# Optimization experiments

Hardware: AMD Instinct MI355X
Metric: run time of the kernel (lower is better)

Reference implementation:

```python
import jax, jax.numpy as jnp
import numpy as np

TEMP = 0.05
DIAG_PENALTY = 1e12
EPS = 1e-8  # matches torch F.cosine_similarity eps


def setup_inputs() -> dict:
    key = jax.random.key(0)
    x = jax.random.normal(key, (8192, 768), dtype=jnp.float32)
    return {"x": x}


def reference(x):
    n = x.shape[0]
    # labels: swap adjacent pairs -> i - (i%2)*2 + 1  (i.e. i XOR 1)
    idx = jnp.arange(n)
    labels = idx - (idx % 2) * 2 + 1
    # cosine similarity matrix via normalize + GEMM (same math as broadcasted
    # F.cosine_similarity: dot(x_i, x_j) / (max(||x_i||,eps) * max(||x_j||,eps)))
    norms = jnp.maximum(jnp.linalg.norm(x, axis=-1, keepdims=True), EPS)
    xn = x / norms
    sim = xn @ xn.T                                   # [N, N]
    sim = sim - jnp.eye(n, dtype=sim.dtype) * DIAG_PENALTY
    logits = sim / TEMP
    # mean cross-entropy with stable log-softmax
    logp = jax.nn.log_softmax(logits, axis=-1)
    loss = -jnp.mean(jnp.take_along_axis(logp, labels[:, None], axis=-1))
    return loss
```

## Files before the change

### kernel.cpp

```cpp
#include <hip/hip_runtime.h>
#include <hip/hip_bf16.h>

#define N 8192
#define D 768
#define TEMP_INV 20.0f
#define NTILES 2080

typedef __attribute__((ext_vector_type(4))) float f32x4;
typedef __attribute__((ext_vector_type(4))) int i32x4;
typedef __attribute__((ext_vector_type(8))) int i32x8;

#define SCALE1 0x7F7F7F7F


__global__ __launch_bounds__(256) void norm_kernel(
    const float* __restrict__ x, unsigned char* __restrict__ xn,
    float* __restrict__ rowsum) {
  int t = threadIdx.x, w = t >> 6, lane = t & 63;
  int p = blockIdx.x;
  __shared__ unsigned int lds[3072];
#pragma unroll
  for (int it = 0; it < 4; ++it) {
    int r = w * 4 + it;
    const float4* xr = (const float4*)(x + (size_t)(p * 16 + r) * D);
    float4 v[3];
    v[0] = xr[lane];
    v[1] = xr[lane + 64];
    v[2] = xr[lane + 128];
    float ss = 0.0f;
#pragma unroll
    for (int i = 0; i < 3; ++i)
      ss += v[i].x * v[i].x + v[i].y * v[i].y + v[i].z * v[i].z + v[i].w * v[i].w;
#pragma unroll
    for (int m = 32; m; m >>= 1) ss += __shfl_xor(ss, m);
    float inv = 1.0f / fmaxf(sqrtf(ss), 1e-8f);
#pragma unroll
    for (int i = 0; i < 3; ++i) {
      int pk = __builtin_amdgcn_cvt_pk_fp8_f32(v[i].x * inv, v[i].y * inv, 0, false);
      pk = __builtin_amdgcn_cvt_pk_fp8_f32(v[i].z * inv, v[i].w * inv, pk, true);
      int d = lane + 64 * i;
      int kc = d >> 5, dd = d & 31;
      int qq = dd >> 3, h = (dd >> 2) & 1, o4 = d & 3;
      lds[kc * 512 + h * 256 + (qq * 16 + r) * 4 + o4] = (unsigned int)pk;
    }
  }
  __syncthreads();
  const uint4* ls = (const uint4*)lds;
  uint4* dst = (uint4*)(xn + (size_t)p * 12288);
#pragma unroll
  for (int j = 0; j < 3; ++j) dst[t + 256 * j] = ls[t + 256 * j];
  if (t < 16) rowsum[p * 16 + t] = 0.0f;
}

__global__ __launch_bounds__(256, 2) void sim_kernel(
    const unsigned char* __restrict__ xn, float* __restrict__ rowsum,
    float* __restrict__ pos) {
  static const short stbase[37] = {
      0, 36, 100, 164, 228, 292, 356, 420,
      484, 520, 584, 648, 712, 776, 840,
      904, 940, 1004, 1068, 1132, 1196,
      1260, 1296, 1360, 1424, 1488,
      1552, 1588, 1652, 1716,
      1780, 1816, 1880,
      1944, 1980,
      2044, 2080};
  static const char sti[36] = {0,0,0,0,0,0,0,0, 1,1,1,1,1,1,1, 2,2,2,2,2,2,
                               3,3,3,3,3, 4,4,4,4, 5,5,5, 6,6, 7};
  static const char stj[36] = {0,1,2,3,4,5,6,7, 1,2,3,4,5,6,7, 2,3,4,5,6,7,
                               3,4,5,6,7, 4,5,6,7, 5,6,7, 6,7, 7};
  int b = blockIdx.x;
  int pp = 260 * (b & 7) + (b >> 3);
  int s = 0;
  while ((int)stbase[s + 1] <= pp) ++s;
  int wofs = pp - stbase[s];
  int SI = sti[s], SJ = stj[s];
  int bi, bj;
  if (SI == SJ) {
    int di = 0, cum = 0;
    while (wofs >= cum + (8 - di)) { cum += 8 - di; ++di; }
    bi = SI * 8 + di;
    bj = SI * 8 + di + (wofs - cum);
  } else {
    bi = SI * 8 + (wofs >> 3);
    bj = SJ * 8 + (wofs & 7);
  }

  int t = threadIdx.x;
  int w = t >> 6, lane = t & 63;
  int q = lane >> 4, cl = lane & 15;
  int wm = w >> 1, wn = w & 1;

  f32x4 acc[4][4] = {};

  const unsigned char* Abase = xn + (size_t)(bi * 8 + wm * 4) * 12288 + lane * 16;
  const unsigned char* Bbase = xn + (size_t)(bj * 8 + wn * 4) * 12288 + lane * 16;

  union Frag { i32x8 v8; struct { i32x4 lo, hi; } pr; };
  Frag a[2][4], bb[2][4];

#define LOAD_KC(buf, kc)                                                   \
  {                                                                        \
    _Pragma("unroll") for (int m = 0; m < 4; ++m) {                        \
      const unsigned char* pA = Abase + m * 12288 + (kc) * 2048;           \
      a[buf][m].pr.lo = *(const i32x4*)pA;                                 \
      a[buf][m].pr.hi = *(const i32x4*)(pA + 1024);                        \
    }                                                                      \
    _Pragma("unroll") for (int n = 0; n < 4; ++n) {                        \
      const unsigned char* pB = Bbase + n * 12288 + (kc) * 2048;           \
      bb[buf][n].pr.lo = *(const i32x4*)pB;                                \
      bb[buf][n].pr.hi = *(const i32x4*)(pB + 1024);                       \
    }                                                                      \
  }

  LOAD_KC(0, 0);
#pragma unroll
  for (int kc = 0; kc < 6; ++kc) {
    int cur = kc & 1;
    if (kc < 5) LOAD_KC(cur ^ 1, kc + 1);
#pragma unroll
    for (int m = 0; m < 4; ++m)
#pragma unroll
      for (int n = 0; n < 4; ++n)
        acc[m][n] = __builtin_amdgcn_mfma_scale_f32_16x16x128_f8f6f4(
            a[cur][m].v8, bb[cur][n].v8, acc[m][n], 0, 0, 0, SCALE1, 0, SCALE1);
  }
#undef LOAD_KC

  int gi0 = bi * 128 + wm * 64;
  int gj0 = bj * 128 + wn * 64;

  float rowp[4][4] = {};
  float colp[4] = {};

  if (bi == bj) {
#pragma unroll
    for (int m = 0; m < 4; ++m)
#pragma unroll
      for (int n = 0; n < 4; ++n)
#pragma unroll
        for (int r = 0; r < 4; ++r) {
          float sv = acc[m][n][r];
          int row = gi0 + m * 16 + q * 4 + r;
          int col = gj0 + n * 16 + cl;
          float e = __expf(TEMP_INV * sv - 20.0f);
          if (col == row) e = 0.0f;
          if (col == (row ^ 1)) pos[row] = TEMP_INV * sv;
          rowp[m][r] += e;
        }
  } else {
#pragma unroll
    for (int m = 0; m < 4; ++m)
#pragma unroll
      for (int n = 0; n < 4; ++n)
#pragma unroll
        for (int r = 0; r < 4; ++r) {
          float e = __expf(TEMP_INV * acc[m][n][r] - 20.0f);
          rowp[m][r] += e;
          colp[n] += e;
        }
  }

#pragma unroll
  for (int m = 0; m < 4; ++m)
#pragma unroll
    for (int r = 0; r < 4; ++r) {
      float v = rowp[m][r];
      v += __shfl_xor(v, 1);
      v += __shfl_xor(v, 2);
      v += __shfl_xor(v, 4);
      v += __shfl_xor(v, 8);
      if (cl == 0) atomicAdd(&rowsum[gi0 + m * 16 + q * 4 + r], v);
    }
  if (bi != bj) {
#pragma unroll
    for (int n = 0; n < 4; ++n) {
      float v = colp[n];
      v += __shfl_xor(v, 16);
      v += __shfl_xor(v, 32);
      if (q == 0) atomicAdd(&rowsum[gj0 + n * 16 + cl], v);
    }
  }
}

__global__ __launch_bounds__(1024) void loss_kernel(
    const float* __restrict__ rowsum, const float* __restrict__ pos,
    float* __restrict__ out) {
  int t = threadIdx.x;
  const float4* r4 = (const float4*)rowsum;
  const float4* p4 = (const float4*)pos;
  float acc = 0.0f;
#pragma unroll
  for (int it = 0; it < 2; ++it) {
    int i = t + it * 1024;
    float4 r = r4[i], pv = p4[i];
    acc += 80.0f + __logf(r.x) + __logf(r.y) + __logf(r.z) + __logf(r.w)
           - pv.x - pv.y - pv.z - pv.w;
  }
#pragma unroll
  for (int m = 32; m; m >>= 1) acc += __shfl_xor(acc, m);
  __shared__ float wsum[16];
  if ((t & 63) == 0) wsum[t >> 6] = acc;
  __syncthreads();
  if (t == 0) {
    float tot = 0.0f;
#pragma unroll
    for (int i = 0; i < 16; ++i) tot += wsum[i];
    out[0] = tot / (float)N;
  }
}

extern "C" void kernel_launch(void* const* d_in, const int* in_sizes, int n_in,
                              void* d_out, int out_size, void* d_ws, size_t ws_size,
                              hipStream_t stream) {
  const float* x = (const float*)d_in[0];
  float* rowsum = (float*)d_ws;
  float* pos = rowsum + N;
  unsigned char* xn = (unsigned char*)(rowsum + 2 * N + 16);

  norm_kernel<<<N / 16, 256, 0, stream>>>(x, xn, rowsum);
  sim_kernel<<<NTILES, 256, 0, stream>>>(xn, rowsum, pos);
  loss_kernel<<<1, 1024, 0, stream>>>(rowsum, pos, (float*)d_out);
}
```

Measured before the change: 133.6 us.

## Use 256x256 LDS-staged tiles for off-diagonal blocks and small diagonal tiles

Replaces the 128x128 register-direct tile scheme with 512-thread blocks that stage fp8 fragments into shared memory through global_load_lds. Off-diagonal blocks now cover 256x256 tiles (496 blocks) and diagonal 256-row bands use 128x128 sub-tiles (96 blocks), 592 blocks in total. The aim is to raise operand reuse per global byte and cut the block count and atomics. The cost is a barrier per k-chunk with no double buffering, larger accumulator register use, and 64KB of LDS per block, which may limit occupancy.

New measurement: 389.3 us. 2.91x slower.

```diff
diff --git a/kernel.cpp b/kernel.cpp
--- a/kernel.cpp
+++ b/kernel.cpp
@@ -4,7 +4,6 @@
 #define N 8192
 #define D 768
 #define TEMP_INV 20.0f
-#define NTILES 2080
 
 typedef __attribute__((ext_vector_type(4))) float f32x4;
 typedef __attribute__((ext_vector_type(4))) int i32x4;
@@ -52,128 +51,186 @@
   if (t < 16) rowsum[p * 16 + t] = 0.0f;
 }
 
-__global__ __launch_bounds__(256, 2) void sim_kernel(
+__global__ __launch_bounds__(512, 2) void sim_kernel(
     const unsigned char* __restrict__ xn, float* __restrict__ rowsum,
     float* __restrict__ pos) {
-  static const short stbase[37] = {
-      0, 36, 100, 164, 228, 292, 356, 420,
-      484, 520, 584, 648, 712, 776, 840,
-      904, 940, 1004, 1068, 1132, 1196,
-      1260, 1296, 1360, 1424, 1488,
-      1552, 1588, 1652, 1716,
-      1780, 1816, 1880,
-      1944, 1980,
-      2044, 2080};
-  static const char sti[36] = {0,0,0,0,0,0,0,0, 1,1,1,1,1,1,1, 2,2,2,2,2,2,
-                               3,3,3,3,3, 4,4,4,4, 5,5,5, 6,6, 7};
-  static const char stj[36] = {0,1,2,3,4,5,6,7, 1,2,3,4,5,6,7, 2,3,4,5,6,7,
-                               3,4,5,6,7, 4,5,6,7, 5,6,7, 6,7, 7};
+  __shared__ __align__(16) unsigned char lds[65536];
+
   int b = blockIdx.x;
-  int pp = 260 * (b & 7) + (b >> 3);
-  int s = 0;
-  while ((int)stbase[s + 1] <= pp) ++s;
-  int wofs = pp - stbase[s];
-  int SI = sti[s], SJ = stj[s];
-  int bi, bj;
-  if (SI == SJ) {
-    int di = 0, cum = 0;
-    while (wofs >= cum + (8 - di)) { cum += 8 - di; ++di; }
-    bi = SI * 8 + di;
-    bj = SI * 8 + di + (wofs - cum);
-  } else {
-    bi = SI * 8 + (wofs >> 3);
-    bj = SJ * 8 + (wofs & 7);
-  }
-
   int t = threadIdx.x;
   int w = t >> 6, lane = t & 63;
   int q = lane >> 4, cl = lane & 15;
-  int wm = w >> 1, wn = w & 1;
-
-  f32x4 acc[4][4] = {};
-
-  const unsigned char* Abase = xn + (size_t)(bi * 8 + wm * 4) * 12288 + lane * 16;
-  const unsigned char* Bbase = xn + (size_t)(bj * 8 + wn * 4) * 12288 + lane * 16;
-
+  int wi = w >> 1, wj = w & 1;
   union Frag { i32x8 v8; struct { i32x4 lo, hi; } pr; };
-  Frag a[2][4], bb[2][4];
-
-#define LOAD_KC(buf, kc)                                                   \
-  {                                                                        \
-    _Pragma("unroll") for (int m = 0; m < 4; ++m) {                        \
-      const unsigned char* pA = Abase + m * 12288 + (kc) * 2048;           \
-      a[buf][m].pr.lo = *(const i32x4*)pA;                                 \
-      a[buf][m].pr.hi = *(const i32x4*)(pA + 1024);                        \
-    }                                                                      \
-    _Pragma("unroll") for (int n = 0; n < 4; ++n) {                        \
-      const unsigned char* pB = Bbase + n * 12288 + (kc) * 2048;           \
-      bb[buf][n].pr.lo = *(const i32x4*)pB;                                \
-      bb[buf][n].pr.hi = *(const i32x4*)(pB + 1024);                       \
-    }                                                                      \
-  }
-
-  LOAD_KC(0, 0);
-#pragma unroll
-  for (int kc = 0; kc < 6; ++kc) {
-    int cur = kc & 1;
-    if (kc < 5) LOAD_KC(cur ^ 1, kc + 1);
+
+  if (b < 96) {
+    int s = (b & 7) * 12 + (b >> 3);
+    int d = s / 3, k = s - 3 * d;
+    int bi = 2 * d + (k == 2);
+    int bj = 2 * d + (k >= 1);
+
+    f32x4 acc[2][4] = {};
+    const unsigned char* Ag = xn + (size_t)(bi * 8) * 12288;
+    const unsigned char* Bg = xn + (size_t)(bj * 8) * 12288;
+
+    for (int kc = 0; kc < 6; ++kc) {
+#pragma unroll
+      for (int r = 0; r < 4; ++r) {
+        int fb = r * 4 + (t >> 7);
+        const unsigned char* src =
+            ((fb < 8) ? (Ag + (size_t)fb * 12288)
+                      : (Bg + (size_t)(fb - 8) * 12288)) +
+            kc * 2048 + (t & 127) * 16;
+        __builtin_amdgcn_global_load_lds(
+            (const __attribute__((address_space(1))) unsigned int*)src,
+            (__attribute__((address_space(3))) unsigned int*)(lds + r * 8192 + t * 16),
+            16, 0, 0);
+      }
+      __syncthreads();
+      Frag a[2];
+#pragma unroll
+      for (int m = 0; m < 2; ++m) {
+        const unsigned char* base = lds + (2 * wi + m) * 2048 + lane * 16;
+        a[m].pr.lo = *(const i32x4*)base;
+        a[m].pr.hi = *(const i32x4*)(base + 1024);
+      }
+#pragma unroll
+      for (int n = 0; n < 4; ++n) {
+        const unsigned char* base = lds + (8 + 4 * wj + n) * 2048 + lane * 16;
+        Frag bf;
+        bf.pr.lo = *(const i32x4*)base;
+        bf.pr.hi = *(const i32x4*)(base + 1024);
+#pragma unroll
+        for (int m = 0; m < 2; ++m)
+          acc[m][n] = __builtin_amdgcn_mfma_scale_f32_16x16x128_f8f6f4(
+              a[m].v8, bf.v8, acc[m][n], 0, 0, 0, SCALE1, 0, SCALE1);
+      }
+      __syncthreads();
+    }
+
+    int gi0 = bi * 128 + wi * 32;
+    int gj0 = bj * 128 + wj * 64;
+    float rowp[2][4] = {};
+    float colp[4] = {};
+    if (bi == bj) {
+#pragma unroll
+      for (int m = 0; m < 2; ++m)
+#pragma unroll
+        for (int n = 0; n < 4; ++n)
+#pragma unroll
+          for (int r = 0; r < 4; ++r) {
+            float sv = acc[m][n][r];
+            int row = gi0 + m * 16 + q * 4 + r;
+            int col = gj0 + n * 16 + cl;
+            float e = __expf(TEMP_INV * sv - 20.0f);
+            if (col == row) e = 0.0f;
+            if (col == (row ^ 1)) pos[row] = TEMP_INV * sv;
+            rowp[m][r] += e;
+          }
+    } else {
+#pragma unroll
+      for (int m = 0; m < 2; ++m)
+#pragma unroll
+        for (int n = 0; n < 4; ++n)
+#pragma unroll
+          for (int r = 0; r < 4; ++r) {
+            float e = __expf(TEMP_INV * acc[m][n][r] - 20.0f);
+            rowp[m][r] += e;
+            colp[n] += e;
+          }
+    }
+#pragma unroll
+    for (int m = 0; m < 2; ++m)
+#pragma unroll
+      for (int r = 0; r < 4; ++r) {
+        float v = rowp[m][r];
+        v += __shfl_xor(v, 1);
+        v += __shfl_xor(v, 2);
+        v += __shfl_xor(v, 4);
+        v += __shfl_xor(v, 8);
+        if (cl == 0) atomicAdd(&rowsum[gi0 + m * 16 + q * 4 + r], v);
+      }
+    if (bi != bj) {
+#pragma unroll
+      for (int n = 0; n < 4; ++n) {
+        float v = colp[n];
+        v += __shfl_xor(v, 16);
+        v += __shfl_xor(v, 32);
+        if (q == 0) atomicAdd(&rowsum[gj0 + n * 16 + cl], v);
+      }
+    }
+  } else {
+    int e = (b & 7) * 62 + ((b - 96) >> 3);
+    int SI = 0, base = 0;
+    while (base + (31 - SI) <= e) { base += 31 - SI; ++SI; }
+    int SJ = SI + 1 + (e - base);
+
+    f32x4 acc[4][8] = {};
+    const unsigned char* Ag = xn + (size_t)(SI * 16) * 12288;
+    const unsigned char* Bg = xn + (size_t)(SJ * 16) * 12288;
+
+    for (int kc = 0; kc < 6; ++kc) {
+#pragma unroll
+      for (int r = 0; r < 8; ++r) {
+        int fb = r * 4 + (t >> 7);
+        const unsigned char* src =
+            ((fb < 16) ? (Ag + (size_t)fb * 12288)
+                       : (Bg + (size_t)(fb - 16) * 12288)) +
+            kc * 2048 + (t & 127) * 16;
+        __builtin_amdgcn_global_load_lds(
+            (const __attribute__((address_space(1))) unsigned int*)src,
+            (__attribute__((address_space(3))) unsigned int*)(lds + r * 8192 + t * 16),
+            16, 0, 0);
+      }
+      __syncthreads();
+      Frag a[4];
+#pragma unroll
+      for (int m = 0; m < 4; ++m) {
+        const unsigned char* bp = lds + (4 * wi + m) * 2048 + lane * 16;
+        a[m].pr.lo = *(const i32x4*)bp;
+        a[m].pr.hi = *(const i32x4*)(bp + 1024);
+      }
+#pragma unroll
+      for (int n = 0; n < 8; ++n) {
+        const unsigned char* bp = lds + (16 + 8 * wj + n) * 2048 + lane * 16;
+        Frag bf;
+        bf.pr.lo = *(const i32x4*)bp;
+        bf.pr.hi = *(const i32x4*)(bp + 1024);
+#pragma unroll
+        for (int m = 0; m < 4; ++m)
+          acc[m][n] = __builtin_amdgcn_mfma_scale_f32_16x16x128_f8f6f4(
+              a[m].v8, bf.v8, acc[m][n], 0, 0, 0, SCALE1, 0, SCALE1);
+      }
+      __syncthreads();
+    }
+
+    int gi0 = SI * 256 + wi * 64;
+    int gj0 = SJ * 256 + wj * 128;
+    float rowp[4][4] = {};
+    float colp[8] = {};
 #pragma unroll
     for (int m = 0; m < 4; ++m)
 #pragma unroll
-      for (int n = 0; n < 4; ++n)
-        acc[m][n] = __builtin_amdgcn_mfma_scale_f32_16x16x128_f8f6f4(
-            a[cur][m].v8, bb[cur][n].v8, acc[m][n], 0, 0, 0, SCALE1, 0, SCALE1);
-  }
-#undef LOAD_KC
-
-  int gi0 = bi * 128 + wm * 64;
-  int gj0 = bj * 128 + wn * 64;
-
-  float rowp[4][4] = {};
-  float colp[4] = {};
-
-  if (bi == bj) {
+      for (int n = 0; n < 8; ++n)
+#pragma unroll
+        for (int r = 0; r < 4; ++r) {
+          float e2 = __expf(TEMP_INV * acc[m][n][r] - 20.0f);
+          rowp[m][r] += e2;
+          colp[n] += e2;
+        }
 #pragma unroll
     for (int m = 0; m < 4; ++m)
 #pragma unroll
-      for (int n = 0; n < 4; ++n)
-#pragma unroll
-        for (int r = 0; r < 4; ++r) {
-          float sv = acc[m][n][r];
-          int row = gi0 + m * 16 + q * 4 + r;
-          int col = gj0 + n * 16 + cl;
-          float e = __expf(TEMP_INV * sv - 20.0f);
-          if (col == row) e = 0.0f;
-          if (col == (row ^ 1)) pos[row] = TEMP_INV * sv;
-          rowp[m][r] += e;
-        }
-  } else {
-#pragma unroll
-    for (int m = 0; m < 4; ++m)
-#pragma unroll
-      for (int n = 0; n < 4; ++n)
-#pragma unroll
-        for (int r = 0; r < 4; ++r) {
-          float e = __expf(TEMP_INV * acc[m][n][r] - 20.0f);
-          rowp[m][r] += e;
-          colp[n] += e;
-        }
-  }
-
-#pragma unroll
-  for (int m = 0; m < 4; ++m)
-#pragma unroll
-    for (int r = 0; r < 4; ++r) {
-      float v = rowp[m][r];
-      v += __shfl_xor(v, 1);
-      v += __shfl_xor(v, 2);
-      v += __shfl_xor(v, 4);
-      v += __shfl_xor(v, 8);
-      if (cl == 0) atomicAdd(&rowsum[gi0 + m * 16 + q * 4 + r], v);
-    }
-  if (bi != bj) {
-#pragma unroll
-    for (int n = 0; n < 4; ++n) {
+      for (int r = 0; r < 4; ++r) {
+        float v = rowp[m][r];
+        v += __shfl_xor(v, 1);
+        v += __shfl_xor(v, 2);
+        v += __shfl_xor(v, 4);
+        v += __shfl_xor(v, 8);
+        if (cl == 0) atomicAdd(&rowsum[gi0 + m * 16 + q * 4 + r], v);
+      }
+#pragma unroll
+    for (int n = 0; n < 8; ++n) {
       float v = colp[n];
       v += __shfl_xor(v, 16);
       v += __shfl_xor(v, 32);
@@ -218,6 +275,6 @@
   unsigned char* xn = (unsigned char*)(rowsum + 2 * N + 16);
 
   norm_kernel<<<N / 16, 256, 0, stream>>>(x, xn, rowsum);
-  sim_kernel<<<NTILES, 256, 0, stream>>>(xn, rowsum, pos);
+  sim_kernel<<<592, 512, 0, stream>>>(xn, rowsum, pos);
   loss_kernel<<<1, 1024, 0, stream>>>(rowsum, pos, (float*)d_out);
 }
```
